# Performance work log

Hardware: AMD Instinct MI355X
Metric: run time of the kernel (lower is better)

The kernel has to match this reference:

```python
import jax, jax.numpy as jnp
import numpy as np

B = 131072
NQ = 5
Z = jnp.array([1.0, -1.0], dtype=jnp.float32)


def _axshape(w):
    return [2 if k == w else 1 for k in range(NQ)]


def _apply_1q(state, U, w):
    # state: (B,2,2,2,2,2) complex64; apply 2x2 gate U on qubit w
    st = jnp.moveaxis(state, 1 + w, -1)
    st = st @ U.T
    return jnp.moveaxis(st, -1, 1 + w)


def _rx(t):
    c = jnp.cos(t / 2)
    s = jnp.sin(t / 2)
    return jnp.stack([jnp.stack([c + 0j, -1j * s]), jnp.stack([-1j * s, c + 0j])]).astype(jnp.complex64)


def _ry(t):
    c = jnp.cos(t / 2)
    s = jnp.sin(t / 2)
    return jnp.stack([jnp.stack([c, -s]), jnp.stack([s, c])]).astype(jnp.complex64)


def _quantum(comb, rw):
    # comb: (B,4). Wires 0,1 <- short feats, wire 2 <- 0, wires 3,4 <- long feats.
    zero = jnp.zeros_like(comb[:, 0])
    angles = [comb[:, 0], comb[:, 1], zero, comb[:, 2], comb[:, 3]]
    # RY(a)|0> = [cos(a/2), sin(a/2)] -> batched product state via einsum (B,32)
    qs = [jnp.stack([jnp.cos(a / 2), jnp.sin(a / 2)], -1).astype(jnp.complex64) for a in angles]
    state = jnp.einsum('bi,bj,bk,bl,bm->bijklm', *qs)
    for layer in range(3):
        for i in range(NQ):
            state = _apply_1q(state, _rx(rw[layer, i, 0]), i)
            state = _apply_1q(state, _ry(rw[layer, i, 1]), i)
        for i in range(NQ):
            for j in range(i + 1, NQ):
                # CNOT(i,j) RZ(th,j) CNOT(i,j) == exp(-i th/2 Z_i Z_j): diagonal phase
                zz = Z.reshape(_axshape(i)) * Z.reshape(_axshape(j))
                phase = jnp.exp((-0.5j) * rw[layer, i, j].astype(jnp.complex64) * zz.astype(jnp.complex64))
                state = state * phase[None]
    probs = jnp.real(state * jnp.conj(state))
    ez = [jnp.sum(probs * Z.reshape(_axshape(w))[None], axis=(1, 2, 3, 4, 5)) for w in range(NQ)]
    return jnp.stack(ez, -1)  # (B,5)


def _forward(x_short, x_long, conv_s_w, conv_s_b, lin_s_w, lin_s_b, conv_l_w, conv_l_b, lin_l_w, lin_l_b, reservoir_weights, readout_w, readout_b):
    dn = ('NCH', 'OIH', 'NCH')
    h = jax.lax.conv_general_dilated(x_short, conv_s_w, (1,), [(1, 1)], dimension_numbers=dn) + conv_s_b[None, :, None]
    feat_s = jax.nn.relu(h).reshape(h.shape[0], -1) @ lin_s_w.T + lin_s_b  # (B,2)
    h = jax.lax.conv_general_dilated(x_long, conv_l_w, (1,), [(2, 2)], dimension_numbers=dn) + conv_l_b[None, :, None]
    h = jax.nn.relu(h)
    h = h.reshape(h.shape[0], 4, 10, 2).max(-1)  # MaxPool1d(2): 20 -> 10
    feat_l = h.reshape(h.shape[0], -1) @ lin_l_w.T + lin_l_b  # (B,2)
    comb = jnp.concatenate([feat_s, feat_l], axis=1)  # (B,4)
    qz = _quantum(comb, reservoir_weights)  # (B,5)
    return qz @ readout_w.T + readout_b  # (B,1)


def setup_inputs() -> dict:
    key = jax.random.key(0)
    ks = jax.random.split(key, 12)
    f32 = jnp.float32
    return {
        'x_short': jax.random.normal(ks[0], (B, 1, 5), f32),
        'x_long': jax.random.normal(ks[1], (B, 1, 20), f32),
        'conv_s_w': jax.random.normal(ks[2], (4, 1, 3), f32) * 0.3,
        'conv_s_b': jax.random.normal(ks[3], (4,), f32) * 0.1,
        'lin_s_w': jax.random.normal(ks[4], (2, 20), f32) * 0.15,
        'lin_s_b': jnp.zeros((2,), f32),
        'conv_l_w': jax.random.normal(ks[5], (4, 1, 5), f32) * 0.3,
        'conv_l_b': jax.random.normal(ks[6], (4,), f32) * 0.1,
        'lin_l_w': jax.random.normal(ks[7], (2, 40), f32) * 0.1,
        'lin_l_b': jnp.zeros((2,), f32),
        'reservoir_weights': jax.random.normal(ks[8], (3, 5, 5), f32),
        'readout_w': jax.random.normal(ks[9], (1, 5), f32) * 0.3,
        'readout_b': jnp.zeros((1,), f32),
    }


def reference(x_short, x_long, conv_s_w, conv_s_b, lin_s_w, lin_s_b, conv_l_w, conv_l_b, lin_l_w, lin_l_b, reservoir_weights, readout_w, readout_b):
    return _forward(x_short, x_long, conv_s_w, conv_s_b, lin_s_w, lin_s_b, conv_l_w, conv_l_b, lin_l_w, lin_l_b, reservoir_weights, readout_w, readout_b)
```

## Files before the change

kernel.cpp:

```cpp
#include <hip/hip_runtime.h>
#include <math.h>


__global__ __launch_bounds__(256) void qcr_prep(
    const float* __restrict__ rw, const float* __restrict__ readout_w,
    const float* __restrict__ readout_b, float* __restrict__ Dout)
{
    __shared__ float s_rxc[15], s_rxs[15], s_ryc[15], s_rys[15];
    __shared__ float s_zzc[96], s_zzs[96], s_coef[32];
    __shared__ float phir[16][33], phii[16][33];
    __shared__ float sA[16][16];
    __shared__ float sC[81];

    const int tid = threadIdx.x;

    if (tid < 15) {
        const int l = tid / 5, i = tid % 5;
        const float tx = rw[l*25 + i*5 + 0] * 0.5f;
        const float ty = rw[l*25 + i*5 + 1] * 0.5f;
        s_rxc[tid] = cosf(tx); s_rxs[tid] = sinf(tx);
        s_ryc[tid] = cosf(ty); s_rys[tid] = sinf(ty);
    }
    if (tid >= 32 && tid < 128) {
        const int e = tid - 32;
        const int l = e >> 5, bi = e & 31;
        float ang = 0.f;
        for (int i = 0; i < 5; ++i) {
            const float si = ((bi >> (4 - i)) & 1) ? -1.f : 1.f;
            for (int j = i + 1; j < 5; ++j) {
                const float sj = ((bi >> (4 - j)) & 1) ? -1.f : 1.f;
                ang += rw[l*25 + i*5 + j] * si * sj;
            }
        }
        ang *= -0.5f;
        s_zzc[e] = cosf(ang); s_zzs[e] = sinf(ang);
    }
    if (tid >= 128 && tid < 160) {
        const int bi = tid - 128;
        float c = 0.f;
        for (int w = 0; w < 5; ++w) {
            const float sw = ((bi >> (4 - w)) & 1) ? -1.f : 1.f;
            c += readout_w[w] * sw;
        }
        s_coef[bi] = c;
    }
    __syncthreads();

    if (tid < 16) {
        float ar[32], ai[32];
        const int P = ((tid & 12) << 1) | (tid & 3);
        #pragma unroll
        for (int idx = 0; idx < 32; ++idx) { ar[idx] = (idx == P) ? 1.f : 0.f; ai[idx] = 0.f; }

        for (int l = 0; l < 3; ++l) {
            #pragma unroll
            for (int qb = 0; qb < 5; ++qb) {
                const float rc = s_rxc[l*5 + qb], rs = s_rxs[l*5 + qb];
                const float yc = s_ryc[l*5 + qb], ys = s_rys[l*5 + qb];
                const int str = 1 << (4 - qb);
                #pragma unroll
                for (int g = 0; g < 16; ++g) {
                    const int i0 = ((g & ~(str - 1)) << 1) | (g & (str - 1));
                    const int i1 = i0 | str;
                    const float a0r = ar[i0], a0i = ai[i0];
                    const float a1r = ar[i1], a1i = ai[i1];
                    const float n0r =  rc*a0r + rs*a1i;
                    const float n0i =  rc*a0i - rs*a1r;
                    const float n1r =  rs*a0i + rc*a1r;
                    const float n1i = -rs*a0r + rc*a1i;
                    ar[i0] = yc*n0r - ys*n1r;
                    ai[i0] = yc*n0i - ys*n1i;
                    ar[i1] = ys*n0r + yc*n1r;
                    ai[i1] = ys*n0i + yc*n1i;
                }
            }
            #pragma unroll
            for (int idx = 0; idx < 32; ++idx) {
                const float pc = s_zzc[l*32 + idx], ps = s_zzs[l*32 + idx];
                const float r = ar[idx]*pc - ai[idx]*ps;
                ai[idx]       = ar[idx]*ps + ai[idx]*pc;
                ar[idx]       = r;
            }
        }
        #pragma unroll
        for (int k = 0; k < 32; ++k) { phir[tid][k] = ar[k]; phii[tid][k] = ai[k]; }
    }
    __syncthreads();

    {
        const int p = tid >> 4, q = tid & 15;
        float acc = 0.f;
        #pragma unroll
        for (int k = 0; k < 32; ++k)
            acc += s_coef[k] * (phir[p][k]*phir[q][k] + phii[p][k]*phii[q][k]);
        sA[p][q] = acc;
    }
    __syncthreads();

    if (tid < 81) {
        const int j0 = tid / 27, j1 = (tid / 9) % 3, j3 = (tid / 3) % 3, j4 = tid % 3;
        const int n0 = 1 + (j0 == 1), n1 = 1 + (j1 == 1);
        const int n3 = 1 + (j3 == 1), n4 = 1 + (j4 == 1);
        float s = 0.f;
        for (int a0 = 0; a0 < n0; ++a0) {
            const int pb0 = (j0 == 2) ? 1 : ((j0 == 1) ? a0 : 0);
            const int qb0 = (j0 == 0) ? 0 : ((j0 == 1) ? 1 - a0 : 1);
            for (int a1 = 0; a1 < n1; ++a1) {
                const int pb1 = (j1 == 2) ? 1 : ((j1 == 1) ? a1 : 0);
                const int qb1 = (j1 == 0) ? 0 : ((j1 == 1) ? 1 - a1 : 1);
                for (int a3 = 0; a3 < n3; ++a3) {
                    const int pb3 = (j3 == 2) ? 1 : ((j3 == 1) ? a3 : 0);
                    const int qb3 = (j3 == 0) ? 0 : ((j3 == 1) ? 1 - a3 : 1);
                    for (int a4 = 0; a4 < n4; ++a4) {
                        const int pb4 = (j4 == 2) ? 1 : ((j4 == 1) ? a4 : 0);
                        const int qb4 = (j4 == 0) ? 0 : ((j4 == 1) ? 1 - a4 : 1);
                        s += sA[(pb0<<3)|(pb1<<2)|(pb3<<1)|pb4]
                               [(qb0<<3)|(qb1<<2)|(qb3<<1)|qb4];
                    }
                }
            }
        }
        sC[tid] = s;
    }
    __syncthreads();

    #pragma unroll
    for (int pass = 0; pass < 4; ++pass) {
        const int P  = (pass == 0) ? 27 : (pass == 1) ? 9 : (pass == 2) ? 3 : 1;
        const int O1 = (pass == 0) ? 9  : 27;
        const int O2 = (pass <= 1) ? 3  : 9;
        const int O3 = (pass <= 2) ? 1  : 3;
        if (tid < 27) {
            const int base = (tid / 9) * O1 + ((tid / 3) % 3) * O2 + (tid % 3) * O3;
            const float v0 = sC[base], v1 = sC[base + P], v2 = sC[base + 2*P];
            sC[base]       = 0.5f * (v0 + v2);
            sC[base + P]   = 0.5f * (v0 - v2);
            sC[base + 2*P] = 0.5f * v1;
        }
        __syncthreads();
    }

    if (tid == 0) sC[0] += readout_b[0];
    __syncthreads();
    if (tid < 81) Dout[tid] = sC[tid];
}

__global__ __launch_bounds__(256) void qcr_main(
    const float* __restrict__ x_short, const float* __restrict__ x_long,
    const float* __restrict__ conv_s_w, const float* __restrict__ conv_s_b,
    const float* __restrict__ lin_s_w,  const float* __restrict__ lin_s_b,
    const float* __restrict__ conv_l_w, const float* __restrict__ conv_l_b,
    const float* __restrict__ lin_l_w,  const float* __restrict__ lin_l_b,
    const float* __restrict__ D, float* __restrict__ out, int nb)
{
    const int b = blockIdx.x * 256 + threadIdx.x;
    if (b >= nb) return;

    float xs[5];
    #pragma unroll
    for (int p = 0; p < 5; ++p) xs[p] = x_short[b*5 + p];

    float f0 = lin_s_b[0], f1 = lin_s_b[1];
    #pragma unroll
    for (int c = 0; c < 4; ++c) {
        #pragma unroll
        for (int p = 0; p < 5; ++p) {
            float h = conv_s_b[c];
            #pragma unroll
            for (int k = 0; k < 3; ++k) {
                const int q = p - 1 + k;
                if (q >= 0 && q < 5) h += conv_s_w[c*3 + k] * xs[q];
            }
            h = fmaxf(h, 0.f);
            f0 += lin_s_w[      c*5 + p] * h;
            f1 += lin_s_w[20 + c*5 + p] * h;
        }
    }

    float xl[20];
    {
        const float4* xl4 = reinterpret_cast<const float4*>(x_long + b*20);
        #pragma unroll
        for (int v = 0; v < 5; ++v) {
            const float4 t = xl4[v];
            xl[4*v+0] = t.x; xl[4*v+1] = t.y; xl[4*v+2] = t.z; xl[4*v+3] = t.w;
        }
    }

    float g0 = lin_l_b[0], g1 = lin_l_b[1];
    #pragma unroll
    for (int c = 0; c < 4; ++c) {
        #pragma unroll
        for (int q = 0; q < 10; ++q) {
            float hm = 0.f;
            #pragma unroll
            for (int t = 0; t < 2; ++t) {
                const int p = 2*q + t;
                float h = conv_l_b[c];
                #pragma unroll
                for (int k = 0; k < 5; ++k) {
                    const int u = p - 2 + k;
                    if (u >= 0 && u < 20) h += conv_l_w[c*5 + k] * xl[u];
                }
                hm = fmaxf(hm, h);
            }
            g0 += lin_l_w[      c*10 + q] * hm;
            g1 += lin_l_w[40 + c*10 + q] * hm;
        }
    }

    float C0, S0, C1, S1, C3, S3, C4, S4;
    sincosf(f0, &S0, &C0);
    sincosf(f1, &S1, &C1);
    sincosf(g0, &S3, &C3);
    sincosf(g1, &S4, &C4);

    float t4[27];
    #pragma unroll
    for (int j = 0; j < 27; ++j)
        t4[j] = D[3*j] + C4 * D[3*j + 1] + S4 * D[3*j + 2];
    float t3[9];
    #pragma unroll
    for (int j = 0; j < 9; ++j)
        t3[j] = t4[3*j] + C3 * t4[3*j + 1] + S3 * t4[3*j + 2];
    float t1[3];
    #pragma unroll
    for (int j = 0; j < 3; ++j)
        t1[j] = t3[3*j] + C1 * t3[3*j + 1] + S1 * t3[3*j + 2];

    out[b] = t1[0] + C0 * t1[1] + S0 * t1[2];
}

extern "C" void kernel_launch(void* const* d_in, const int* in_sizes, int n_in,
                              void* d_out, int out_size, void* d_ws, size_t ws_size,
                              hipStream_t stream) {
    const float* x_short    = (const float*)d_in[0];
    const float* x_long     = (const float*)d_in[1];
    const float* conv_s_w   = (const float*)d_in[2];
    const float* conv_s_b   = (const float*)d_in[3];
    const float* lin_s_w    = (const float*)d_in[4];
    const float* lin_s_b    = (const float*)d_in[5];
    const float* conv_l_w   = (const float*)d_in[6];
    const float* conv_l_b   = (const float*)d_in[7];
    const float* lin_l_w    = (const float*)d_in[8];
    const float* lin_l_b    = (const float*)d_in[9];
    const float* rw         = (const float*)d_in[10];
    const float* readout_w  = (const float*)d_in[11];
    const float* readout_b  = (const float*)d_in[12];
    float* out = (float*)d_out;
    float* Dws = (float*)d_ws;

    const int nb = in_sizes[0] / 5;

    hipLaunchKernelGGL(qcr_prep, dim3(1), dim3(256), 0, stream,
                       rw, readout_w, readout_b, Dws);
    hipLaunchKernelGGL(qcr_main, dim3((nb + 255) / 256), dim3(256), 0, stream,
                       x_short, x_long, conv_s_w, conv_s_b, lin_s_w, lin_s_b,
                       conv_l_w, conv_l_b, lin_l_w, lin_l_b, Dws, out, nb);
}
```

Baseline: 100.2 us.

## Fuse prep into main kernel and parallelize state simulation across lanes

Merges the single-block prep kernel into the batch kernel so every block recomputes the 81-entry coefficient table in shared memory, removing a kernel launch and the global round-trip. The state-vector simulation is split across 16 lanes per basis column, with cross-lane shuffles for gate pairs instead of 16 serial threads each holding 32 complex amplitudes. In exchange, all 512 blocks now repeat the reservoir precompute and its several barriers before doing per-sample work.

```diff
diff --git a/kernel.cpp b/kernel.cpp
--- a/kernel.cpp
+++ b/kernel.cpp
@@ -2,9 +2,14 @@
 #include <math.h>
 
 
-__global__ __launch_bounds__(256) void qcr_prep(
-    const float* __restrict__ rw, const float* __restrict__ readout_w,
-    const float* __restrict__ readout_b, float* __restrict__ Dout)
+__global__ __launch_bounds__(256) void qcr_fused(
+    const float* __restrict__ x_short, const float* __restrict__ x_long,
+    const float* __restrict__ conv_s_w, const float* __restrict__ conv_s_b,
+    const float* __restrict__ lin_s_w,  const float* __restrict__ lin_s_b,
+    const float* __restrict__ conv_l_w, const float* __restrict__ conv_l_b,
+    const float* __restrict__ lin_l_w,  const float* __restrict__ lin_l_b,
+    const float* __restrict__ rw,       const float* __restrict__ readout_w,
+    const float* __restrict__ readout_b, float* __restrict__ out, int nb)
 {
     __shared__ float s_rxc[15], s_rxs[15], s_ryc[15], s_rys[15];
     __shared__ float s_zzc[96], s_zzs[96], s_coef[32];
@@ -46,44 +51,64 @@
     }
     __syncthreads();
 
-    if (tid < 16) {
-        float ar[32], ai[32];
-        const int P = ((tid & 12) << 1) | (tid & 3);
-        #pragma unroll
-        for (int idx = 0; idx < 32; ++idx) { ar[idx] = (idx == P) ? 1.f : 0.f; ai[idx] = 0.f; }
+    {
+        const int p = tid >> 4;
+        const int t = tid & 15;
+        const int P = ((p & 12) << 1) | (p & 3);
+
+        float lr = (t == P)      ? 1.f : 0.f, li = 0.f;
+        float hr = (t + 16 == P) ? 1.f : 0.f, hi2 = 0.f;
 
         for (int l = 0; l < 3; ++l) {
             #pragma unroll
             for (int qb = 0; qb < 5; ++qb) {
                 const float rc = s_rxc[l*5 + qb], rs = s_rxs[l*5 + qb];
                 const float yc = s_ryc[l*5 + qb], ys = s_rys[l*5 + qb];
-                const int str = 1 << (4 - qb);
-                #pragma unroll
-                for (int g = 0; g < 16; ++g) {
-                    const int i0 = ((g & ~(str - 1)) << 1) | (g & (str - 1));
-                    const int i1 = i0 | str;
-                    const float a0r = ar[i0], a0i = ai[i0];
-                    const float a1r = ar[i1], a1i = ai[i1];
-                    const float n0r =  rc*a0r + rs*a1i;
-                    const float n0i =  rc*a0i - rs*a1r;
-                    const float n1r =  rs*a0i + rc*a1r;
-                    const float n1i = -rs*a0r + rc*a1i;
-                    ar[i0] = yc*n0r - ys*n1r;
-                    ai[i0] = yc*n0i - ys*n1i;
-                    ar[i1] = ys*n0r + yc*n1r;
-                    ai[i1] = ys*n0i + yc*n1i;
+                if (qb == 0) {
+                    const float n0r =  rc*lr  + rs*hi2;
+                    const float n0i =  rc*li  - rs*hr;
+                    const float n1r =  rs*li  + rc*hr;
+                    const float n1i = -rs*lr  + rc*hi2;
+                    lr  = yc*n0r - ys*n1r;  li  = yc*n0i - ys*n1i;
+                    hr  = ys*n0r + yc*n1r;  hi2 = ys*n0i + yc*n1i;
+                } else {
+                    const int str = 1 << (4 - qb);
+                    const bool up = (t & str) != 0;
+                    float pr = __shfl_xor(lr, str, 64);
+                    float pi = __shfl_xor(li, str, 64);
+                    {
+                        const float a0r = up ? pr : lr,  a0i = up ? pi : li;
+                        const float a1r = up ? lr : pr,  a1i = up ? li : pi;
+                        const float n0r =  rc*a0r + rs*a1i;
+                        const float n0i =  rc*a0i - rs*a1r;
+                        const float n1r =  rs*a0i + rc*a1r;
+                        const float n1i = -rs*a0r + rc*a1i;
+                        lr = up ? (ys*n0r + yc*n1r) : (yc*n0r - ys*n1r);
+                        li = up ? (ys*n0i + yc*n1i) : (yc*n0i - ys*n1i);
+                    }
+                    pr = __shfl_xor(hr,  str, 64);
+                    pi = __shfl_xor(hi2, str, 64);
+                    {
+                        const float a0r = up ? pr : hr,  a0i = up ? pi : hi2;
+                        const float a1r = up ? hr : pr,  a1i = up ? hi2 : pi;
+                        const float n0r =  rc*a0r + rs*a1i;
+                        const float n0i =  rc*a0i - rs*a1r;
+                        const float n1r =  rs*a0i + rc*a1r;
+                        const float n1i = -rs*a0r + rc*a1i;
+                        hr  = up ? (ys*n0r + yc*n1r) : (yc*n0r - ys*n1r);
+                        hi2 = up ? (ys*n0i + yc*n1i) : (yc*n0i - ys*n1i);
+                    }
                 }
             }
-            #pragma unroll
-            for (int idx = 0; idx < 32; ++idx) {
-                const float pc = s_zzc[l*32 + idx], ps = s_zzs[l*32 + idx];
-                const float r = ar[idx]*pc - ai[idx]*ps;
-                ai[idx]       = ar[idx]*ps + ai[idx]*pc;
-                ar[idx]       = r;
-            }
-        }
-        #pragma unroll
-        for (int k = 0; k < 32; ++k) { phir[tid][k] = ar[k]; phii[tid][k] = ai[k]; }
+            {
+                float pc = s_zzc[l*32 + t], ps = s_zzs[l*32 + t];
+                float r  = lr*pc - li*ps;  li = lr*ps + li*pc;  lr = r;
+                pc = s_zzc[l*32 + t + 16]; ps = s_zzs[l*32 + t + 16];
+                r  = hr*pc - hi2*ps;  hi2 = hr*ps + hi2*pc;  hr = r;
+            }
+        }
+        phir[p][t]      = lr;  phii[p][t]      = li;
+        phir[p][t + 16] = hr;  phii[p][t + 16] = hi2;
     }
     __syncthreads();
 
@@ -139,21 +164,10 @@
         }
         __syncthreads();
     }
-
     if (tid == 0) sC[0] += readout_b[0];
     __syncthreads();
-    if (tid < 81) Dout[tid] = sC[tid];
-}
-
-__global__ __launch_bounds__(256) void qcr_main(
-    const float* __restrict__ x_short, const float* __restrict__ x_long,
-    const float* __restrict__ conv_s_w, const float* __restrict__ conv_s_b,
-    const float* __restrict__ lin_s_w,  const float* __restrict__ lin_s_b,
-    const float* __restrict__ conv_l_w, const float* __restrict__ conv_l_b,
-    const float* __restrict__ lin_l_w,  const float* __restrict__ lin_l_b,
-    const float* __restrict__ D, float* __restrict__ out, int nb)
-{
-    const int b = blockIdx.x * 256 + threadIdx.x;
+
+    const int b = blockIdx.x * 256 + tid;
     if (b >= nb) return;
 
     float xs[5];
@@ -218,7 +232,7 @@
     float t4[27];
     #pragma unroll
     for (int j = 0; j < 27; ++j)
-        t4[j] = D[3*j] + C4 * D[3*j + 1] + S4 * D[3*j + 2];
+        t4[j] = sC[3*j] + C4 * sC[3*j + 1] + S4 * sC[3*j + 2];
     float t3[9];
     #pragma unroll
     for (int j = 0; j < 9; ++j)
@@ -248,13 +262,11 @@
     const float* readout_w  = (const float*)d_in[11];
     const float* readout_b  = (const float*)d_in[12];
     float* out = (float*)d_out;
-    float* Dws = (float*)d_ws;
 
     const int nb = in_sizes[0] / 5;
-
-    hipLaunchKernelGGL(qcr_prep, dim3(1), dim3(256), 0, stream,
-                       rw, readout_w, readout_b, Dws);
-    hipLaunchKernelGGL(qcr_main, dim3((nb + 255) / 256), dim3(256), 0, stream,
+    dim3 grid((nb + 255) / 256), block(256);
+    hipLaunchKernelGGL(qcr_fused, grid, block, 0, stream,
                        x_short, x_long, conv_s_w, conv_s_b, lin_s_w, lin_s_b,
-                       conv_l_w, conv_l_b, lin_l_w, lin_l_b, Dws, out, nb);
+                       conv_l_w, conv_l_b, lin_l_w, lin_l_b, rw, readout_w,
+                       readout_b, out, nb);
 }
```

New measurement: 95.83 us. 4.3% less time.
